# Kernel optimization log

Hardware: AMD Instinct MI355X
Metric: run time of the kernel (lower is better)

The kernel has to match this reference:

```python
import jax, jax.numpy as jnp
import numpy as np
import math

H = W = 512
N_ANGLES = 180
TOTAL_ANGLES = 180.0
DIAG = int(math.ceil(math.sqrt(2.0) * max(H, W)))  # 725
PW = (DIAG - W) // 2  # 106
PH = (DIAG - H) // 2  # 106
P = W + 2 * PW        # 724 (torch F.pad arithmetic)


def setup_inputs() -> dict:
    key = jax.random.key(0)
    x = jax.random.normal(key, (H, W), dtype=jnp.float32)
    return {"x": x}


def _bilinear_sample_zeros(img, ix, iy):
    """grid_sample(align_corners=False, padding_mode='zeros') on a single [P,P] img.
    ix, iy: [N,P,P] pixel-space sample coords. Returns [N,P,P]."""
    n = img.shape[0]
    x0 = jnp.floor(ix)
    y0 = jnp.floor(iy)
    wx = ix - x0
    wy = iy - y0
    x0i = x0.astype(jnp.int32)
    y0i = y0.astype(jnp.int32)
    x1i = x0i + 1
    y1i = y0i + 1

    def g(yi, xi):
        v = img[jnp.clip(yi, 0, n - 1), jnp.clip(xi, 0, n - 1)]
        m = (yi >= 0) & (yi < n) & (xi >= 0) & (xi < n)
        return v * m.astype(img.dtype)

    return (g(y0i, x0i) * (1 - wx) * (1 - wy)
            + g(y0i, x1i) * wx * (1 - wy)
            + g(y1i, x0i) * (1 - wx) * wy
            + g(y1i, x1i) * wx * wy)


def reference(x):
    # pad image to (near-)diagonal square, matching torch F.pad semantics
    padded = jnp.pad(x, ((PH, PH), (PW, PW)))  # [P, P]

    angles_deg = jnp.linspace(0.0, TOTAL_ANGLES, N_ANGLES)
    ang = angles_deg * (jnp.pi / 180.0)
    c = jnp.cos(ang)[:, None, None]
    s = jnp.sin(ang)[:, None, None]

    # affine_grid normalized coords, align_corners=False: t = (2k+1)/P - 1
    t = (2.0 * jnp.arange(P, dtype=jnp.float32) + 1.0) / P - 1.0
    Xn = t[None, None, :]  # output x (width)
    Yn = t[None, :, None]  # output y (height)

    # theta = [[cos, -sin, 0],[sin, cos, 0]]
    xs = c * Xn - s * Yn   # [N,P,P] normalized sample x
    ys = s * Xn + c * Yn

    # unnormalize (align_corners=False)
    ix = ((xs + 1.0) * P - 1.0) * 0.5
    iy = ((ys + 1.0) * P - 1.0) * 0.5

    rotated = _bilinear_sample_zeros(padded, ix, iy)  # [N,P,P]
    # sinogram = rotated.squeeze(1).sum(dim=2) -> sum over last (width) axis
    sinogram = rotated.sum(axis=2)  # [N, P]
    return sinogram, rotated[:, None, :, :]
```

## Files before the change

kernel.cpp:

```cpp
#include <hip/hip_runtime.h>
#include <math.h>

#define N_ANGLES 180
#define P 724
#define W_IN 512


__global__ __launch_bounds__(256) void prep_trig(float2* __restrict__ sc) {
    int a = threadIdx.x;
    if (a < N_ANGLES) {
        float deg = (float)a * (180.0f / 179.0f);
        float ang = deg * (float)(M_PI / 180.0);
        sc[a] = make_float2(cosf(ang), sinf(ang));
    }
}

__global__ __launch_bounds__(256) void prep_transpose(const float* __restrict__ in,
                                                      float* __restrict__ out) {
    __shared__ float tile[32][33];
    const int bx = blockIdx.x * 32, by = blockIdx.y * 32;
    const int tx = threadIdx.x, ty = threadIdx.y;
    #pragma unroll
    for (int r = 0; r < 32; r += 8)
        tile[ty + r][tx] = in[(by + ty + r) * W_IN + bx + tx];
    __syncthreads();
    #pragma unroll
    for (int r = 0; r < 32; r += 8)
        out[(bx + ty + r) * W_IN + by + tx] = tile[tx][ty + r];
}

template <int MODE>
__global__ __launch_bounds__(256) void radon_kernel(
    const float* __restrict__ x,
    const float2* __restrict__ sc,
    const float* __restrict__ xT,
    float* __restrict__ sino,
    float* __restrict__ rot)
{
    const int block = blockIdx.x;
    const int a = block / P;
    const int i = block - a * P;
    const int tid = threadIdx.x;

    float c, s;
    if (MODE > 0) {
        float2 cs = sc[a];
        c = cs.x; s = cs.y;
    } else {
        float deg = (float)a * (180.0f / 179.0f);
        float ang = deg * (float)(M_PI / 180.0);
        c = cosf(ang); s = sinf(ang);
    }

    const float fi = (float)i - 361.5f;
    const float Kx = 255.5f - 361.5f * c - s * fi;
    const float Ky = 255.5f - 361.5f * s + c * fi;

    const bool useT = (MODE == 2) && (fabsf(s) > fabsf(c));
    const float* __restrict__ bimg = useT ? xT : x;

    float* rrow = rot + (size_t)block * P;
    float lsum = 0.0f;

    #pragma unroll
    for (int k = 0; k < 3; ++k) {
        const int j = tid + (k << 8);
        if (j < P) {
            const float jf = (float)j;
            const float ix = fmaf(jf, c, Kx);
            const float iy = fmaf(jf, s, Ky);
            const float x0f = floorf(ix);
            const float y0f = floorf(iy);
            const int x0 = (int)x0f;
            const int y0 = (int)y0f;
            const int x1 = x0 + 1;
            const int y1 = y0 + 1;

            float val = 0.0f;
            const bool outp = ((unsigned)x1 > 512u) || ((unsigned)y1 > 512u);
            if (!__all((int)outp)) {
                float wx1 = ix - x0f, wy1 = iy - y0f;
                float wx0 = 1.0f - wx1, wy0 = 1.0f - wy1;

                const bool inp = ((unsigned)x0 < 511u) && ((unsigned)y0 < 511u);
                if (__all((int)inp)) {
                    const int rr = useT ? x0 : y0;
                    const int cc = useT ? y0 : x0;
                    const float* bp = bimg + (rr << 9) + cc;
                    const float v00 = bp[0];
                    const float vA  = bp[1];
                    const float vB  = bp[512];
                    const float v11 = bp[513];
                    const float u0 = useT ? wy0 : wx0;
                    const float u1 = useT ? wy1 : wx1;
                    const float q0 = useT ? wx0 : wy0;
                    const float q1 = useT ? wx1 : wy1;
                    val = fmaf(q1, fmaf(u1, v11, u0 * vB),
                               q0 * fmaf(u1, vA, u0 * v00));
                } else {
                    wx0 = ((unsigned)x0 < 512u) ? wx0 : 0.0f;
                    wx1 = ((unsigned)x1 < 512u) ? wx1 : 0.0f;
                    wy0 = ((unsigned)y0 < 512u) ? wy0 : 0.0f;
                    wy1 = ((unsigned)y1 < 512u) ? wy1 : 0.0f;
                    const int xc0 = min(max(x0, 0), 511);
                    const int xc1 = min(max(x1, 0), 511);
                    const int yc0 = min(max(y0, 0), 511);
                    const int yc1 = min(max(y1, 0), 511);
                    const int r0 = useT ? xc0 : yc0;
                    const int r1 = useT ? xc1 : yc1;
                    const int c0 = useT ? yc0 : xc0;
                    const int c1 = useT ? yc1 : xc1;
                    const float v00 = bimg[(r0 << 9) + c0];
                    const float vA  = bimg[(r0 << 9) + c1];
                    const float vB  = bimg[(r1 << 9) + c0];
                    const float v11 = bimg[(r1 << 9) + c1];
                    const float u0 = useT ? wy0 : wx0;
                    const float u1 = useT ? wy1 : wx1;
                    const float q0 = useT ? wx0 : wy0;
                    const float q1 = useT ? wx1 : wy1;
                    val = fmaf(q1, fmaf(u1, v11, u0 * vB),
                               q0 * fmaf(u1, vA, u0 * v00));
                }
            }
            __builtin_nontemporal_store(val, &rrow[j]);
            lsum += val;
        }
    }

    for (int off = 32; off > 0; off >>= 1)
        lsum += __shfl_down(lsum, off, 64);

    __shared__ float ws_red[4];
    const int lane = tid & 63;
    const int wid  = tid >> 6;
    if (lane == 0) ws_red[wid] = lsum;
    __syncthreads();
    if (tid == 0)
        sino[block] = ws_red[0] + ws_red[1] + ws_red[2] + ws_red[3];
}


extern "C" void kernel_launch(void* const* d_in, const int* in_sizes, int n_in,
                              void* d_out, int out_size, void* d_ws, size_t ws_size,
                              hipStream_t stream) {
    const float* x = (const float*)d_in[0];
    float* sino = (float*)d_out;
    float* rot  = sino + (size_t)N_ANGLES * P;
    float* ws   = (float*)d_ws;

    const dim3 grid(N_ANGLES * P), blk(256);
    if (ws && ws_size >= (size_t)(512 + 512 * 512) * sizeof(float)) {
        float* xT = ws + 512;
        prep_trig<<<dim3(1), dim3(256), 0, stream>>>((float2*)ws);
        prep_transpose<<<dim3(16, 16), dim3(32, 8), 0, stream>>>(x, xT);
        radon_kernel<2><<<grid, blk, 0, stream>>>(x, (const float2*)ws, xT, sino, rot);
    } else if (ws && ws_size >= (size_t)512 * sizeof(float)) {
        prep_trig<<<dim3(1), dim3(256), 0, stream>>>((float2*)ws);
        radon_kernel<1><<<grid, blk, 0, stream>>>(x, (const float2*)ws, nullptr, sino, rot);
    } else {
        radon_kernel<0><<<grid, blk, 0, stream>>>(x, nullptr, nullptr, sino, rot);
    }
}
```

Before: 442.1 us.

## Vectorize rotated-row stores, clip sampling to valid range, merge prep kernels

Each thread now produces four consecutive outputs and writes them with one 128-bit nontemporal store, using 192-thread blocks that exactly cover a 724-wide row. An analytic per-row interval of sample positions that can touch the image is computed, and groups outside it skip sampling and just store zeros. The trig table computation is merged into the transpose kernel to drop a launch. Per-thread register use rises from the four-wide unrolled sampling, and the fallback mode now calls the transpose with a null output pointer.

```diff
diff --git a/kernel.cpp b/kernel.cpp
--- a/kernel.cpp
+++ b/kernel.cpp
@@ -5,32 +5,35 @@
 #define P 724
 #define W_IN 512
 
+typedef float vfloat4 __attribute__((ext_vector_type(4)));
 
-__global__ __launch_bounds__(256) void prep_trig(float2* __restrict__ sc) {
-    int a = threadIdx.x;
-    if (a < N_ANGLES) {
-        float deg = (float)a * (180.0f / 179.0f);
-        float ang = deg * (float)(M_PI / 180.0);
-        sc[a] = make_float2(cosf(ang), sinf(ang));
-    }
-}
-
-__global__ __launch_bounds__(256) void prep_transpose(const float* __restrict__ in,
-                                                      float* __restrict__ out) {
+__global__ __launch_bounds__(256) void prep_all(const float* __restrict__ in,
+                                                float* __restrict__ outT,
+                                                float2* __restrict__ sc) {
     __shared__ float tile[32][33];
     const int bx = blockIdx.x * 32, by = blockIdx.y * 32;
     const int tx = threadIdx.x, ty = threadIdx.y;
+
+    if (bx == 0 && by == 0) {
+        int t = ty * 32 + tx;
+        if (t < N_ANGLES) {
+            float deg = (float)t * (180.0f / 179.0f);
+            float ang = deg * (float)(M_PI / 180.0);
+            sc[t] = make_float2(cosf(ang), sinf(ang));
+        }
+    }
+
     #pragma unroll
     for (int r = 0; r < 32; r += 8)
         tile[ty + r][tx] = in[(by + ty + r) * W_IN + bx + tx];
     __syncthreads();
     #pragma unroll
     for (int r = 0; r < 32; r += 8)
-        out[(bx + ty + r) * W_IN + by + tx] = tile[tx][ty + r];
+        outT[(bx + ty + r) * W_IN + by + tx] = tile[tx][ty + r];
 }
 
 template <int MODE>
-__global__ __launch_bounds__(256) void radon_kernel(
+__global__ __launch_bounds__(192) void radon_kernel(
     const float* __restrict__ x,
     const float2* __restrict__ sc,
     const float* __restrict__ xT,
@@ -58,85 +61,109 @@
 
     const bool useT = (MODE == 2) && (fabsf(s) > fabsf(c));
     const float* __restrict__ bimg = useT ? xT : x;
+    const float fcoef = useT ? s : c;
+    const float fK    = useT ? Ky : Kx;
+    const float scoef = useT ? c : s;
+    const float sK    = useT ? Kx : Ky;
+
+    float lo = 0.0f, hi = 723.0f;
+    bool empty = false;
+    {
+        if (fabsf(c) >= 1e-3f) {
+            float rc = 1.0f / c;
+            float b1 = (-1.0f - Kx) * rc, b2 = (512.0f - Kx) * rc;
+            lo = fmaxf(lo, fminf(b1, b2)); hi = fminf(hi, fmaxf(b1, b2));
+        } else if (Kx <= -1.0f || Kx >= 512.0f) empty = true;
+        if (fabsf(s) >= 1e-3f) {
+            float rs = 1.0f / s;
+            float b1 = (-1.0f - Ky) * rs, b2 = (512.0f - Ky) * rs;
+            lo = fmaxf(lo, fminf(b1, b2)); hi = fminf(hi, fmaxf(b1, b2));
+        } else if (Ky <= -1.0f || Ky >= 512.0f) empty = true;
+    }
+    int jlo, jhi;
+    if (empty || lo > hi) { jlo = 1; jhi = 0; }
+    else {
+        jlo = max(0, (int)floorf(lo) - 2);
+        jhi = min(723, (int)ceilf(hi) + 2);
+    }
 
     float* rrow = rot + (size_t)block * P;
     float lsum = 0.0f;
 
-    #pragma unroll
-    for (int k = 0; k < 3; ++k) {
-        const int j = tid + (k << 8);
-        if (j < P) {
-            const float jf = (float)j;
-            const float ix = fmaf(jf, c, Kx);
-            const float iy = fmaf(jf, s, Ky);
-            const float x0f = floorf(ix);
-            const float y0f = floorf(iy);
-            const int x0 = (int)x0f;
-            const int y0 = (int)y0f;
-            const int x1 = x0 + 1;
-            const int y1 = y0 + 1;
+    if (tid < 181) {
+        const int j0 = tid << 2;
+        vfloat4 o;
+        if (j0 + 3 < jlo || j0 > jhi) {
+            o = (vfloat4){0.0f, 0.0f, 0.0f, 0.0f};
+        } else {
+            const float jf = (float)j0;
+            float fcv[4], scv[4];
+            fcv[0] = fmaf(jf, fcoef, fK);
+            scv[0] = fmaf(jf, scoef, sK);
+            #pragma unroll
+            for (int d = 1; d < 4; ++d) { fcv[d] = fcv[d-1] + fcoef; scv[d] = scv[d-1] + scoef; }
 
-            float val = 0.0f;
-            const bool outp = ((unsigned)x1 > 512u) || ((unsigned)y1 > 512u);
-            if (!__all((int)outp)) {
-                float wx1 = ix - x0f, wy1 = iy - y0f;
-                float wx0 = 1.0f - wx1, wy0 = 1.0f - wy1;
+            float f0f[4], s0f[4];
+            int f0i[4], s0i[4];
+            bool interior = true;
+            #pragma unroll
+            for (int d = 0; d < 4; ++d) {
+                f0f[d] = floorf(fcv[d]); s0f[d] = floorf(scv[d]);
+                f0i[d] = (int)f0f[d];    s0i[d] = (int)s0f[d];
+                interior = interior && ((unsigned)f0i[d] < 511u) && ((unsigned)s0i[d] < 511u);
+            }
 
-                const bool inp = ((unsigned)x0 < 511u) && ((unsigned)y0 < 511u);
-                if (__all((int)inp)) {
-                    const int rr = useT ? x0 : y0;
-                    const int cc = useT ? y0 : x0;
-                    const float* bp = bimg + (rr << 9) + cc;
-                    const float v00 = bp[0];
-                    const float vA  = bp[1];
-                    const float vB  = bp[512];
-                    const float v11 = bp[513];
-                    const float u0 = useT ? wy0 : wx0;
-                    const float u1 = useT ? wy1 : wx1;
-                    const float q0 = useT ? wx0 : wy0;
-                    const float q1 = useT ? wx1 : wy1;
-                    val = fmaf(q1, fmaf(u1, v11, u0 * vB),
-                               q0 * fmaf(u1, vA, u0 * v00));
-                } else {
-                    wx0 = ((unsigned)x0 < 512u) ? wx0 : 0.0f;
-                    wx1 = ((unsigned)x1 < 512u) ? wx1 : 0.0f;
-                    wy0 = ((unsigned)y0 < 512u) ? wy0 : 0.0f;
-                    wy1 = ((unsigned)y1 < 512u) ? wy1 : 0.0f;
-                    const int xc0 = min(max(x0, 0), 511);
-                    const int xc1 = min(max(x1, 0), 511);
-                    const int yc0 = min(max(y0, 0), 511);
-                    const int yc1 = min(max(y1, 0), 511);
-                    const int r0 = useT ? xc0 : yc0;
-                    const int r1 = useT ? xc1 : yc1;
-                    const int c0 = useT ? yc0 : xc0;
-                    const int c1 = useT ? yc1 : xc1;
-                    const float v00 = bimg[(r0 << 9) + c0];
-                    const float vA  = bimg[(r0 << 9) + c1];
-                    const float vB  = bimg[(r1 << 9) + c0];
-                    const float v11 = bimg[(r1 << 9) + c1];
-                    const float u0 = useT ? wy0 : wx0;
-                    const float u1 = useT ? wy1 : wx1;
-                    const float q0 = useT ? wx0 : wy0;
-                    const float q1 = useT ? wx1 : wy1;
-                    val = fmaf(q1, fmaf(u1, v11, u0 * vB),
-                               q0 * fmaf(u1, vA, u0 * v00));
+            float v[4];
+            if (__all((int)interior)) {
+                #pragma unroll
+                for (int d = 0; d < 4; ++d) {
+                    const float wf1 = fcv[d] - f0f[d], wf0 = 1.0f - wf1;
+                    const float ws1 = scv[d] - s0f[d], ws0 = 1.0f - ws1;
+                    const float* bp = bimg + (s0i[d] << 9) + f0i[d];
+                    const float v00 = bp[0],   vA = bp[1];
+                    const float vB  = bp[512], v11 = bp[513];
+                    v[d] = fmaf(ws1, fmaf(wf1, v11, wf0 * vB),
+                                ws0 * fmaf(wf1, vA, wf0 * v00));
+                }
+            } else {
+                #pragma unroll
+                for (int d = 0; d < 4; ++d) {
+                    const int fa = f0i[d], fb = fa + 1;
+                    const int sa = s0i[d], sb = sa + 1;
+                    float wf1 = fcv[d] - f0f[d], wf0 = 1.0f - wf1;
+                    float ws1 = scv[d] - s0f[d], ws0 = 1.0f - ws1;
+                    wf0 = ((unsigned)fa < 512u) ? wf0 : 0.0f;
+                    wf1 = ((unsigned)fb < 512u) ? wf1 : 0.0f;
+                    ws0 = ((unsigned)sa < 512u) ? ws0 : 0.0f;
+                    ws1 = ((unsigned)sb < 512u) ? ws1 : 0.0f;
+                    const int fca = min(max(fa, 0), 511);
+                    const int fcb = min(max(fb, 0), 511);
+                    const int sca = min(max(sa, 0), 511);
+                    const int scb = min(max(sb, 0), 511);
+                    const float v00 = bimg[(sca << 9) + fca];
+                    const float v01 = bimg[(sca << 9) + fcb];
+                    const float v10 = bimg[(scb << 9) + fca];
+                    const float v11 = bimg[(scb << 9) + fcb];
+                    v[d] = fmaf(ws1, fmaf(wf1, v11, wf0 * v10),
+                                ws0 * fmaf(wf1, v01, wf0 * v00));
                 }
             }
-            __builtin_nontemporal_store(val, &rrow[j]);
-            lsum += val;
+            o = (vfloat4){v[0], v[1], v[2], v[3]};
         }
+        __builtin_nontemporal_store(o, (vfloat4*)(rrow + j0));
+        lsum = (o.x + o.y) + (o.z + o.w);
     }
 
     for (int off = 32; off > 0; off >>= 1)
         lsum += __shfl_down(lsum, off, 64);
 
-    __shared__ float ws_red[4];
+    __shared__ float ws_red[3];
     const int lane = tid & 63;
     const int wid  = tid >> 6;
     if (lane == 0) ws_red[wid] = lsum;
     __syncthreads();
     if (tid == 0)
-        sino[block] = ws_red[0] + ws_red[1] + ws_red[2] + ws_red[3];
+        sino[block] = ws_red[0] + ws_red[1] + ws_red[2];
 }
 
 
@@ -148,14 +175,13 @@
     float* rot  = sino + (size_t)N_ANGLES * P;
     float* ws   = (float*)d_ws;
 
-    const dim3 grid(N_ANGLES * P), blk(256);
+    const dim3 grid(N_ANGLES * P), blk(192);
     if (ws && ws_size >= (size_t)(512 + 512 * 512) * sizeof(float)) {
         float* xT = ws + 512;
-        prep_trig<<<dim3(1), dim3(256), 0, stream>>>((float2*)ws);
-        prep_transpose<<<dim3(16, 16), dim3(32, 8), 0, stream>>>(x, xT);
+        prep_all<<<dim3(16, 16), dim3(32, 8), 0, stream>>>(x, xT, (float2*)ws);
         radon_kernel<2><<<grid, blk, 0, stream>>>(x, (const float2*)ws, xT, sino, rot);
     } else if (ws && ws_size >= (size_t)512 * sizeof(float)) {
-        prep_trig<<<dim3(1), dim3(256), 0, stream>>>((float2*)ws);
+        prep_all<<<dim3(16, 16), dim3(32, 8), 0, stream>>>(x, nullptr, (float2*)ws);
         radon_kernel<1><<<grid, blk, 0, stream>>>(x, (const float2*)ws, nullptr, sino, rot);
     } else {
         radon_kernel<0><<<grid, blk, 0, stream>>>(x, nullptr, nullptr, sino, rot);
```

Result: slower. 513.0 us (+16.0%).
